# Kernel tuning notes

Hardware: AMD Instinct MI355X
Metric: run time of the kernel (lower is better)

The kernel has to match this reference:

```python
import jax, jax.numpy as jnp
import numpy as np

NUM_GRAPHS = 128
NODES_PER_GRAPH = 512
N_NODES = NUM_GRAPHS * NODES_PER_GRAPH
N_EDGES = 524288
IN_DIM = 128
HID = 128
OUT_DIM = 10
N_LAYERS = 3
POOL_RATIO = 0.5  # TopKPooling default ratio


def setup_inputs() -> dict:
    key = jax.random.key(0)
    ks = jax.random.split(key, 16)
    x = jax.random.normal(ks[0], (N_NODES, IN_DIM), dtype=jnp.float32)
    edge_index = jax.random.randint(ks[1], (2, N_EDGES), 0, N_NODES, dtype=jnp.int64)
    batch = jnp.repeat(jnp.arange(NUM_GRAPHS, dtype=jnp.int64), NODES_PER_GRAPH)
    s = 0.05
    return {
        "x": x,
        "edge_index": edge_index,
        "batch": batch,
        "emb_W": jax.random.normal(ks[2], (IN_DIM, HID), dtype=jnp.float32) * s,
        "emb_b": jnp.zeros((HID,), dtype=jnp.float32),
        "gcn_W": jax.random.normal(ks[3], (N_LAYERS, HID, HID), dtype=jnp.float32) * s,
        "gcn_b": jnp.zeros((N_LAYERS, HID), dtype=jnp.float32),
        "pool_p": jax.random.normal(ks[4], (HID,), dtype=jnp.float32),
        "fc1_W": jax.random.normal(ks[5], (HID, 128), dtype=jnp.float32) * s,
        "fc1_b": jnp.zeros((128,), dtype=jnp.float32),
        "fc2_W": jax.random.normal(ks[6], (128, 64), dtype=jnp.float32) * s,
        "fc2_b": jnp.zeros((64,), dtype=jnp.float32),
        "fc3_W": jax.random.normal(ks[7], (64, OUT_DIM), dtype=jnp.float32) * s,
        "fc3_b": jnp.zeros((OUT_DIM,), dtype=jnp.float32),
    }


def reference(x, edge_index, batch, emb_W, emb_b, gcn_W, gcn_b, pool_p,
              fc1_W, fc1_b, fc2_W, fc2_b, fc3_W, fc3_b):
    n = x.shape[0]
    # embedding
    h = x @ emb_W + emb_b
    # GCNConv normalization (PyG semantics): add self loops, deg from target scatter
    loop = jnp.arange(n, dtype=edge_index.dtype)
    src = jnp.concatenate([edge_index[0], loop])
    dst = jnp.concatenate([edge_index[1], loop])
    deg = jax.ops.segment_sum(jnp.ones_like(src, dtype=h.dtype), dst, num_segments=n)
    dinv = jnp.where(deg > 0, jax.lax.rsqrt(jnp.maximum(deg, 1e-12)), 0.0)
    norm = dinv[src] * dinv[dst]  # [E+n]
    for l in range(gcn_W.shape[0]):
        hw = h @ gcn_W[l]                                   # [n, HID]
        msg = hw[src] * norm[:, None]                        # gather + scale
        h = jax.nn.relu(jax.ops.segment_sum(msg, dst, num_segments=n) + gcn_b[l])
    # TopKPooling (ratio=0.5, tanh nonlinearity), uniform graphs -> reshape + top_k
    npg = n // NUM_GRAPHS
    k = int(np.ceil(POOL_RATIO * npg))
    score = (h @ pool_p) / jnp.linalg.norm(pool_p)           # [n]
    score_g = score.reshape(NUM_GRAPHS, npg)
    topv, topi = jax.lax.top_k(score_g, k)                   # [G, k]
    h_g = h.reshape(NUM_GRAPHS, npg, -1)
    h_sel = jnp.take_along_axis(h_g, topi[:, :, None], axis=1) * jnp.tanh(topv)[:, :, None]
    pooled = h_sel.mean(axis=1)                              # global_mean_pool -> [G, HID]
    # MLP head (dropout is identity in eval)
    z = jax.nn.relu(pooled @ fc1_W + fc1_b)
    z = jax.nn.relu(z @ fc2_W + fc2_b)
    return z @ fc3_W + fc3_b
```

## Files before the change

kernel.cpp:

```cpp
#include <hip/hip_runtime.h>
#include <hip/hip_bf16.h>
#include <math.h>


static __device__ __forceinline__ float4 f4add(float4 a, float4 b) {
    return make_float4(a.x + b.x, a.y + b.y, a.z + b.z, a.w + b.w);
}
static __device__ __forceinline__ float4 f4fma(float s, float4 a, float4 acc) {
    return make_float4(fmaf(s, a.x, acc.x), fmaf(s, a.y, acc.y),
                       fmaf(s, a.z, acc.z), fmaf(s, a.w, acc.w));
}

__global__ __launch_bounds__(128) void fold_emb(
    const float* __restrict__ embW, const float* __restrict__ embb,
    const float* __restrict__ W0, float* __restrict__ W01,
    float* __restrict__ b01)
{
    const int r = blockIdx.x;
    const int c = threadIdx.x;
    __shared__ float rs[128];
    rs[c] = (r < 128) ? embW[r * 128 + c] : embb[c];
    __syncthreads();
    float s = 0.f;
#pragma unroll 8
    for (int k = 0; k < 128; k++) s = fmaf(rs[k], W0[k * 128 + c], s);
    if (r < 128) W01[r * 128 + c] = s;
    else         b01[c] = s;
}

#define ASTRIDE 260
#define WSTRIDE 140
__global__ __launch_bounds__(256) void gemm128(
    const float* __restrict__ A, const float* __restrict__ W,
    const float* __restrict__ bias, const float* __restrict__ rowscale,
    float* __restrict__ out, int n)
{
    __shared__ float As[32 * ASTRIDE];
    __shared__ float Ws[32 * WSTRIDE];
    const int tid  = threadIdx.x;
    const int rb   = blockIdx.x * 256;
    const int tc   = tid & 15;
    const int tr   = tid >> 4;
    const int colg = tc * 8;
    const int cswz = colg + ((colg >> 5) << 2);
    const int rowg = tr * 16;

    const int a_kq = tid & 7;
    const int a_r0 = tid >> 3;
    const int w_c  = (tid & 31) * 4;
    const int w_cs = w_c + ((w_c >> 5) << 2);
    const int w_k  = tid >> 5;

    float acc[16][8];
#pragma unroll
    for (int i = 0; i < 16; i++)
#pragma unroll
        for (int j = 0; j < 8; j++) acc[i][j] = 0.f;

    float4 areg[8], wreg[4];
#pragma unroll
    for (int t = 0; t < 8; t++)
        areg[t] = *(const float4*)&A[(size_t)(rb + t * 32 + a_r0) * 128 + a_kq * 4];
#pragma unroll
    for (int t = 0; t < 4; t++)
        wreg[t] = *(const float4*)&W[(size_t)(t * 8 + w_k) * 128 + w_c];

#pragma unroll 1
    for (int k0 = 0; k0 < 128; k0 += 32) {
#pragma unroll
        for (int t = 0; t < 8; t++) {
            const int m = t * 32 + a_r0;
            const float4 av = areg[t];
            As[(a_kq * 4 + 0) * ASTRIDE + m] = av.x;
            As[(a_kq * 4 + 1) * ASTRIDE + m] = av.y;
            As[(a_kq * 4 + 2) * ASTRIDE + m] = av.z;
            As[(a_kq * 4 + 3) * ASTRIDE + m] = av.w;
        }
#pragma unroll
        for (int t = 0; t < 4; t++)
            *(float4*)&Ws[(t * 8 + w_k) * WSTRIDE + w_cs] = wreg[t];
        __syncthreads();
        if (k0 < 96) {
#pragma unroll
            for (int t = 0; t < 8; t++)
                areg[t] = *(const float4*)&A[(size_t)(rb + t * 32 + a_r0) * 128 + k0 + 32 + a_kq * 4];
#pragma unroll
            for (int t = 0; t < 4; t++)
                wreg[t] = *(const float4*)&W[(size_t)(k0 + 32 + t * 8 + w_k) * 128 + w_c];
        }
#pragma unroll 8
        for (int kk = 0; kk < 32; kk++) {
            const float* ar = &As[kk * ASTRIDE + rowg];
            float4 a0 = *(const float4*)&ar[0];
            float4 a1 = *(const float4*)&ar[4];
            float4 a2 = *(const float4*)&ar[8];
            float4 a3 = *(const float4*)&ar[12];
            float4 b0 = *(const float4*)&Ws[kk * WSTRIDE + cswz];
            float4 b1 = *(const float4*)&Ws[kk * WSTRIDE + cswz + 4];
            float av[16] = {a0.x, a0.y, a0.z, a0.w, a1.x, a1.y, a1.z, a1.w,
                            a2.x, a2.y, a2.z, a2.w, a3.x, a3.y, a3.z, a3.w};
            float bv[8]  = {b0.x, b0.y, b0.z, b0.w, b1.x, b1.y, b1.z, b1.w};
#pragma unroll
            for (int i = 0; i < 16; i++)
#pragma unroll
                for (int j = 0; j < 8; j++) acc[i][j] = fmaf(av[i], bv[j], acc[i][j]);
        }
        __syncthreads();
    }

    float4 bb0 = make_float4(0.f, 0.f, 0.f, 0.f), bb1 = bb0;
    if (bias) {
        bb0 = *(const float4*)&bias[colg];
        bb1 = *(const float4*)&bias[colg + 4];
    }
#pragma unroll
    for (int i = 0; i < 16; i++) {
        const int row  = rb + rowg + i;
        const float sc = rowscale ? rowscale[row] : 1.f;
        float4 o0, o1;
        o0.x = (acc[i][0] + bb0.x) * sc;  o0.y = (acc[i][1] + bb0.y) * sc;
        o0.z = (acc[i][2] + bb0.z) * sc;  o0.w = (acc[i][3] + bb0.w) * sc;
        o1.x = (acc[i][4] + bb1.x) * sc;  o1.y = (acc[i][5] + bb1.y) * sc;
        o1.z = (acc[i][6] + bb1.z) * sc;  o1.w = (acc[i][7] + bb1.w) * sc;
        *(float4*)&out[(size_t)row * 128 + colg]     = o0;
        *(float4*)&out[(size_t)row * 128 + colg + 4] = o1;
    }
}

__global__ void count_edges(const int* __restrict__ dst, int* __restrict__ cnt, int E)
{
    int e = blockIdx.x * blockDim.x + threadIdx.x;
    if (e < E) atomicAdd(&cnt[dst[e]], 1);
}

__global__ void dinv_k(const int* __restrict__ cnt, float* __restrict__ dinv, int n)
{
    int i = blockIdx.x * blockDim.x + threadIdx.x;
    if (i < n) dinv[i] = rsqrtf((float)(cnt[i] + 1));
}

__global__ void scan1(const int* __restrict__ cnt, int* __restrict__ offs,
                      int* __restrict__ bsum)
{
    __shared__ int tmp[256];
    int t = threadIdx.x;
    int i = blockIdx.x * 256 + t;
    int v = cnt[i];
    tmp[t] = v;
    __syncthreads();
    for (int o = 1; o < 256; o <<= 1) {
        int add = (t >= o) ? tmp[t - o] : 0;
        __syncthreads();
        tmp[t] += add;
        __syncthreads();
    }
    offs[i] = tmp[t] - v;
    if (t == 255) bsum[blockIdx.x] = tmp[255];
}

__global__ void scan2(const int* __restrict__ bsum, int* __restrict__ boff)
{
    __shared__ int tmp[256];
    int t = threadIdx.x;
    int v = bsum[t];
    tmp[t] = v;
    __syncthreads();
    for (int o = 1; o < 256; o <<= 1) {
        int add = (t >= o) ? tmp[t - o] : 0;
        __syncthreads();
        tmp[t] += add;
        __syncthreads();
    }
    boff[t] = tmp[t] - v;
}

__global__ void scan3(int* __restrict__ offs, const int* __restrict__ boff,
                      int* __restrict__ cursor, int n, int E)
{
    int i = blockIdx.x * 256 + threadIdx.x;
    int v = offs[i] + boff[blockIdx.x];
    offs[i]   = v;
    cursor[i] = v;
    if (i == 0) offs[n] = E;
}

__global__ void scatter_edges(const int* __restrict__ src, const int* __restrict__ dst,
                              int* __restrict__ cursor, int* __restrict__ csr, int E)
{
    int e = blockIdx.x * blockDim.x + threadIdx.x;
    if (e < E) {
        int d   = dst[e];
        int pos = atomicAdd(&cursor[d], 1);
        csr[pos] = src[e];
    }
}

__global__ __launch_bounds__(256) void aggregate(
    const float* __restrict__ hs, const int* __restrict__ csr,
    const int* __restrict__ offs, const float* __restrict__ dinv,
    const float* __restrict__ bias, float* __restrict__ hout,
    const float* __restrict__ pool_p, float* __restrict__ scores, int n)
{
    const int grp  = threadIdx.x >> 5;
    const int lane = threadIdx.x & 31;
    const int node = blockIdx.x * 8 + grp;
    const float4* __restrict__ hv = (const float4*)hs;

    const int e0 = offs[node], e1 = offs[node + 1];

    int   ix[16];
    float mk[16];
#pragma unroll
    for (int j = 0; j < 16; j++) {
        const int  e  = e0 + j;
        const bool v  = e < e1;
        const int  ce = v ? e : (e1 > 0 ? e1 - 1 : 0);
        ix[j] = csr[ce];
        mk[j] = v ? 1.f : 0.f;
    }

    float4 a0 = hv[(size_t)node * 32 + lane];
    float4 a1 = make_float4(0.f, 0.f, 0.f, 0.f);
    float4 a2 = a1, a3 = a1;

#pragma unroll
    for (int b = 0; b < 2; b++) {
        float4 r[8];
#pragma unroll
        for (int j = 0; j < 8; j++)
            r[j] = hv[(size_t)ix[b * 8 + j] * 32 + lane];
        a0 = f4fma(mk[b * 8 + 0], r[0], a0);
        a1 = f4fma(mk[b * 8 + 1], r[1], a1);
        a2 = f4fma(mk[b * 8 + 2], r[2], a2);
        a3 = f4fma(mk[b * 8 + 3], r[3], a3);
        a0 = f4fma(mk[b * 8 + 4], r[4], a0);
        a1 = f4fma(mk[b * 8 + 5], r[5], a1);
        a2 = f4fma(mk[b * 8 + 6], r[6], a2);
        a3 = f4fma(mk[b * 8 + 7], r[7], a3);
    }
    for (int e = e0 + 16; e < e1; e++) {
        a1 = f4add(a1, hv[(size_t)csr[e] * 32 + lane]);
    }

    float4 s = f4add(f4add(a0, a1), f4add(a2, a3));
    const float dv = dinv[node];
    const float4 bb = ((const float4*)bias)[lane];
    float4 o;
    o.x = fmaxf(fmaf(s.x, dv, bb.x), 0.f);
    o.y = fmaxf(fmaf(s.y, dv, bb.y), 0.f);
    o.z = fmaxf(fmaf(s.z, dv, bb.z), 0.f);
    o.w = fmaxf(fmaf(s.w, dv, bb.w), 0.f);
    ((float4*)hout)[(size_t)node * 32 + lane] = o;

    if (scores) {
        float4 pv = ((const float4*)pool_p)[lane];
        float d  = o.x * pv.x + o.y * pv.y + o.z * pv.z + o.w * pv.w;
        float nn = pv.x * pv.x + pv.y * pv.y + pv.z * pv.z + pv.w * pv.w;
#pragma unroll
        for (int off = 16; off > 0; off >>= 1) {
            d  += __shfl_xor(d, off);
            nn += __shfl_xor(nn, off);
        }
        if (lane == 0) scores[node] = d * rsqrtf(nn);
    }
}

__global__ __launch_bounds__(512) void topk_pool(
    const float* __restrict__ scores, const float* __restrict__ h,
    float* __restrict__ pooled)
{
    __shared__ float s[512];
    __shared__ int   sel[256];
    __shared__ float w[256];
    __shared__ float4 red[512];
    const int g = blockIdx.x;
    const int i = threadIdx.x;
    s[i] = scores[g * 512 + i];
    __syncthreads();
    float si = s[i];
    int rank = 0;
    for (int j = 0; j < 512; j++) {
        float sj = s[j];
        rank += (sj > si) || (sj == si && j < i);
    }
    if (rank < 256) {
        sel[rank] = i;
        w[rank]   = tanhf(si) * (1.f / 256.f);
    }
    __syncthreads();
    const int c   = (i & 31) * 4;
    const int grp = i >> 5;
    float4 acc = make_float4(0.f, 0.f, 0.f, 0.f);
    for (int t = grp; t < 256; t += 16) {
        float wt  = w[t];
        int   idx = sel[t];
        float4 r = *(const float4*)&h[((size_t)g * 512 + idx) * 128 + c];
        acc = f4fma(wt, r, acc);
    }
    red[i] = acc;
    __syncthreads();
    if (i < 256) red[i] = f4add(red[i], red[i + 256]);
    __syncthreads();
    if (i < 128) red[i] = f4add(red[i], red[i + 128]);
    __syncthreads();
    if (i < 64) red[i] = f4add(red[i], red[i + 64]);
    __syncthreads();
    if (i < 32) {
        float4 v = f4add(red[i], red[i + 32]);
        *(float4*)&pooled[g * 128 + i * 4] = v;
    }
}

__global__ __launch_bounds__(128) void mlp_head(
    const float* __restrict__ pooled,
    const float* __restrict__ fc1W, const float* __restrict__ fc1b,
    const float* __restrict__ fc2W, const float* __restrict__ fc2b,
    const float* __restrict__ fc3W, const float* __restrict__ fc3b,
    float* __restrict__ out)
{
    __shared__ float pld[128];
    __shared__ float z1[128];
    __shared__ float z2[64];
    int g = blockIdx.x, j = threadIdx.x;
    pld[j] = pooled[g * 128 + j];
    __syncthreads();
    float a = fc1b[j];
    for (int k = 0; k < 128; k++) a += pld[k] * fc1W[k * 128 + j];
    z1[j] = fmaxf(a, 0.f);
    __syncthreads();
    if (j < 64) {
        float b = fc2b[j];
        for (int k = 0; k < 128; k++) b += z1[k] * fc2W[k * 64 + j];
        z2[j] = fmaxf(b, 0.f);
    }
    __syncthreads();
    if (j < 10) {
        float o = fc3b[j];
        for (int k = 0; k < 64; k++) o += z2[k] * fc3W[k * 10 + j];
        out[g * 10 + j] = o;
    }
}

extern "C" void kernel_launch(void* const* d_in, const int* in_sizes, int n_in,
                              void* d_out, int out_size, void* d_ws, size_t ws_size,
                              hipStream_t stream)
{
    const float* x     = (const float*)d_in[0];
    const int*   eidx  = (const int*)d_in[1];
    const float* embW  = (const float*)d_in[3];
    const float* embb  = (const float*)d_in[4];
    const float* gcnW  = (const float*)d_in[5];
    const float* gcnb  = (const float*)d_in[6];
    const float* poolp = (const float*)d_in[7];
    const float* fc1W  = (const float*)d_in[8];
    const float* fc1b  = (const float*)d_in[9];
    const float* fc2W  = (const float*)d_in[10];
    const float* fc2b  = (const float*)d_in[11];
    const float* fc3W  = (const float*)d_in[12];
    const float* fc3b  = (const float*)d_in[13];
    float* out = (float*)d_out;

    const int n = in_sizes[0] / 128;
    const int E = in_sizes[1] / 2;
    const int G = n / 512;

    const int* src = eidx;
    const int* dst = eidx + E;

    char* ws = (char*)d_ws;
    size_t off = 0;
    auto carve = [&](size_t bytes) {
        void* p = ws + off;
        off += (bytes + 255) & ~(size_t)255;
        return p;
    };
    float* h      = (float*)carve((size_t)n * 128 * 4);
    float* hs     = (float*)carve((size_t)n * 128 * 4);
    float* dinv   = (float*)carve((size_t)n * 4);
    int*   cnt    = (int*)carve((size_t)n * 4);
    int*   offs   = (int*)carve((size_t)(n + 1) * 4);
    int*   cursor = (int*)carve((size_t)n * 4);
    int*   bsum   = (int*)carve(256 * 4);
    int*   boff   = (int*)carve(256 * 4);
    int*   csr    = (int*)carve((size_t)E * 4);
    float* scores = (float*)carve((size_t)n * 4);
    float* pooled = (float*)carve((size_t)G * 128 * 4);
    float* W01    = (float*)carve(128 * 128 * 4);
    float* b01    = (float*)carve(128 * 4);
    (void)ws_size;

    hipMemsetAsync(cnt, 0, (size_t)n * 4, stream);
    count_edges<<<E / 256, 256, 0, stream>>>(dst, cnt, E);
    dinv_k<<<n / 256, 256, 0, stream>>>(cnt, dinv, n);
    scan1<<<n / 256, 256, 0, stream>>>(cnt, offs, bsum);
    scan2<<<1, 256, 0, stream>>>(bsum, boff);
    scan3<<<n / 256, 256, 0, stream>>>(offs, boff, cursor, n, E);
    scatter_edges<<<E / 256, 256, 0, stream>>>(src, dst, cursor, csr, E);

    fold_emb<<<129, 128, 0, stream>>>(embW, embb, gcnW, W01, b01);

    gemm128<<<n / 256, 256, 0, stream>>>(x, W01, b01, dinv, hs, n);
    aggregate<<<n / 8, 256, 0, stream>>>(hs, csr, offs, dinv, gcnb, h,
                                         poolp, nullptr, n);

    for (int l = 1; l < 3; l++) {
        gemm128<<<n / 256, 256, 0, stream>>>(h, gcnW + (size_t)l * 128 * 128,
                                             nullptr, dinv, hs, n);
        aggregate<<<n / 8, 256, 0, stream>>>(
            hs, csr, offs, dinv, gcnb + (size_t)l * 128, h,
            poolp, (l == 2) ? scores : nullptr, n);
    }

    topk_pool<<<G, 512, 0, stream>>>(scores, h, pooled);
    mlp_head<<<G, 128, 0, stream>>>(pooled, fc1W, fc1b, fc2W, fc2b, fc3W, fc3b, out);
}
```

Baseline: 436.0 us.

## Halve GEMM row tile, fuse dinv into scan, and batch all aggregate gathers

The node GEMM tile drops from 256 to 128 rows per block, with 8x8 accumulators per thread, which doubles the block count and cuts register pressure for better occupancy and load balance. The A-tile LDS stride changes to 257, so the float4 LDS reads are no longer 16-byte aligned and may be split or rely on unaligned LDS support. The separate dinv kernel is folded into scan1, removing one launch and one read of the degree array. The aggregate kernel now issues all 16 neighbour gathers before any accumulation, raising memory-level parallelism at the cost of more live registers.

```diff
diff --git a/kernel.cpp b/kernel.cpp
--- a/kernel.cpp
+++ b/kernel.cpp
@@ -28,7 +28,7 @@
     else         b01[c] = s;
 }
 
-#define ASTRIDE 260
+#define ASTRIDE 257
 #define WSTRIDE 140
 __global__ __launch_bounds__(256) void gemm128(
     const float* __restrict__ A, const float* __restrict__ W,
@@ -38,29 +38,29 @@
     __shared__ float As[32 * ASTRIDE];
     __shared__ float Ws[32 * WSTRIDE];
     const int tid  = threadIdx.x;
-    const int rb   = blockIdx.x * 256;
+    const int rb   = blockIdx.x * 128;
     const int tc   = tid & 15;
     const int tr   = tid >> 4;
     const int colg = tc * 8;
     const int cswz = colg + ((colg >> 5) << 2);
-    const int rowg = tr * 16;
+    const int rowg = tr * 8;
 
     const int a_kq = tid & 7;
-    const int a_r0 = tid >> 3;
+    const int a_m  = tid >> 3;
     const int w_c  = (tid & 31) * 4;
     const int w_cs = w_c + ((w_c >> 5) << 2);
     const int w_k  = tid >> 5;
 
-    float acc[16][8];
-#pragma unroll
-    for (int i = 0; i < 16; i++)
+    float acc[8][8];
+#pragma unroll
+    for (int i = 0; i < 8; i++)
 #pragma unroll
         for (int j = 0; j < 8; j++) acc[i][j] = 0.f;
 
-    float4 areg[8], wreg[4];
-#pragma unroll
-    for (int t = 0; t < 8; t++)
-        areg[t] = *(const float4*)&A[(size_t)(rb + t * 32 + a_r0) * 128 + a_kq * 4];
+    float4 areg[4], wreg[4];
+#pragma unroll
+    for (int t = 0; t < 4; t++)
+        areg[t] = *(const float4*)&A[(size_t)(rb + t * 32 + a_m) * 128 + a_kq * 4];
 #pragma unroll
     for (int t = 0; t < 4; t++)
         wreg[t] = *(const float4*)&W[(size_t)(t * 8 + w_k) * 128 + w_c];
@@ -68,8 +68,8 @@
 #pragma unroll 1
     for (int k0 = 0; k0 < 128; k0 += 32) {
 #pragma unroll
-        for (int t = 0; t < 8; t++) {
-            const int m = t * 32 + a_r0;
+        for (int t = 0; t < 4; t++) {
+            const int m = t * 32 + a_m;
             const float4 av = areg[t];
             As[(a_kq * 4 + 0) * ASTRIDE + m] = av.x;
             As[(a_kq * 4 + 1) * ASTRIDE + m] = av.y;
@@ -82,26 +82,22 @@
         __syncthreads();
         if (k0 < 96) {
 #pragma unroll
-            for (int t = 0; t < 8; t++)
-                areg[t] = *(const float4*)&A[(size_t)(rb + t * 32 + a_r0) * 128 + k0 + 32 + a_kq * 4];
+            for (int t = 0; t < 4; t++)
+                areg[t] = *(const float4*)&A[(size_t)(rb + t * 32 + a_m) * 128 + k0 + 32 + a_kq * 4];
 #pragma unroll
             for (int t = 0; t < 4; t++)
                 wreg[t] = *(const float4*)&W[(size_t)(k0 + 32 + t * 8 + w_k) * 128 + w_c];
         }
 #pragma unroll 8
         for (int kk = 0; kk < 32; kk++) {
-            const float* ar = &As[kk * ASTRIDE + rowg];
-            float4 a0 = *(const float4*)&ar[0];
-            float4 a1 = *(const float4*)&ar[4];
-            float4 a2 = *(const float4*)&ar[8];
-            float4 a3 = *(const float4*)&ar[12];
+            float4 a0 = *(const float4*)&As[kk * ASTRIDE + rowg];
+            float4 a1 = *(const float4*)&As[kk * ASTRIDE + rowg + 4];
             float4 b0 = *(const float4*)&Ws[kk * WSTRIDE + cswz];
             float4 b1 = *(const float4*)&Ws[kk * WSTRIDE + cswz + 4];
-            float av[16] = {a0.x, a0.y, a0.z, a0.w, a1.x, a1.y, a1.z, a1.w,
-                            a2.x, a2.y, a2.z, a2.w, a3.x, a3.y, a3.z, a3.w};
-            float bv[8]  = {b0.x, b0.y, b0.z, b0.w, b1.x, b1.y, b1.z, b1.w};
-#pragma unroll
-            for (int i = 0; i < 16; i++)
+            float av[8] = {a0.x, a0.y, a0.z, a0.w, a1.x, a1.y, a1.z, a1.w};
+            float bv[8] = {b0.x, b0.y, b0.z, b0.w, b1.x, b1.y, b1.z, b1.w};
+#pragma unroll
+            for (int i = 0; i < 8; i++)
 #pragma unroll
                 for (int j = 0; j < 8; j++) acc[i][j] = fmaf(av[i], bv[j], acc[i][j]);
         }
@@ -114,7 +110,7 @@
         bb1 = *(const float4*)&bias[colg + 4];
     }
 #pragma unroll
-    for (int i = 0; i < 16; i++) {
+    for (int i = 0; i < 8; i++) {
         const int row  = rb + rowg + i;
         const float sc = rowscale ? rowscale[row] : 1.f;
         float4 o0, o1;
@@ -133,19 +129,14 @@
     if (e < E) atomicAdd(&cnt[dst[e]], 1);
 }
 
-__global__ void dinv_k(const int* __restrict__ cnt, float* __restrict__ dinv, int n)
-{
-    int i = blockIdx.x * blockDim.x + threadIdx.x;
-    if (i < n) dinv[i] = rsqrtf((float)(cnt[i] + 1));
-}
-
 __global__ void scan1(const int* __restrict__ cnt, int* __restrict__ offs,
-                      int* __restrict__ bsum)
+                      int* __restrict__ bsum, float* __restrict__ dinv)
 {
     __shared__ int tmp[256];
     int t = threadIdx.x;
     int i = blockIdx.x * 256 + t;
     int v = cnt[i];
+    dinv[i] = rsqrtf((float)(v + 1));
     tmp[t] = v;
     __syncthreads();
     for (int o = 1; o < 256; o <<= 1) {
@@ -219,24 +210,22 @@
         mk[j] = v ? 1.f : 0.f;
     }
 
-    float4 a0 = hv[(size_t)node * 32 + lane];
+    float4 self = hv[(size_t)node * 32 + lane];
+    float4 r[16];
+#pragma unroll
+    for (int j = 0; j < 16; j++)
+        r[j] = hv[(size_t)ix[j] * 32 + lane];
+    asm volatile("" ::: "memory");
+
+    float4 a0 = self;
     float4 a1 = make_float4(0.f, 0.f, 0.f, 0.f);
     float4 a2 = a1, a3 = a1;
-
-#pragma unroll
-    for (int b = 0; b < 2; b++) {
-        float4 r[8];
-#pragma unroll
-        for (int j = 0; j < 8; j++)
-            r[j] = hv[(size_t)ix[b * 8 + j] * 32 + lane];
-        a0 = f4fma(mk[b * 8 + 0], r[0], a0);
-        a1 = f4fma(mk[b * 8 + 1], r[1], a1);
-        a2 = f4fma(mk[b * 8 + 2], r[2], a2);
-        a3 = f4fma(mk[b * 8 + 3], r[3], a3);
-        a0 = f4fma(mk[b * 8 + 4], r[4], a0);
-        a1 = f4fma(mk[b * 8 + 5], r[5], a1);
-        a2 = f4fma(mk[b * 8 + 6], r[6], a2);
-        a3 = f4fma(mk[b * 8 + 7], r[7], a3);
+#pragma unroll
+    for (int j = 0; j < 16; j += 4) {
+        a0 = f4fma(mk[j + 0], r[j + 0], a0);
+        a1 = f4fma(mk[j + 1], r[j + 1], a1);
+        a2 = f4fma(mk[j + 2], r[j + 2], a2);
+        a3 = f4fma(mk[j + 3], r[j + 3], a3);
     }
     for (int e = e0 + 16; e < e1; e++) {
         a1 = f4add(a1, hv[(size_t)csr[e] * 32 + lane]);
@@ -391,20 +380,19 @@
 
     hipMemsetAsync(cnt, 0, (size_t)n * 4, stream);
     count_edges<<<E / 256, 256, 0, stream>>>(dst, cnt, E);
-    dinv_k<<<n / 256, 256, 0, stream>>>(cnt, dinv, n);
-    scan1<<<n / 256, 256, 0, stream>>>(cnt, offs, bsum);
+    scan1<<<n / 256, 256, 0, stream>>>(cnt, offs, bsum, dinv);
     scan2<<<1, 256, 0, stream>>>(bsum, boff);
     scan3<<<n / 256, 256, 0, stream>>>(offs, boff, cursor, n, E);
     scatter_edges<<<E / 256, 256, 0, stream>>>(src, dst, cursor, csr, E);
 
     fold_emb<<<129, 128, 0, stream>>>(embW, embb, gcnW, W01, b01);
 
-    gemm128<<<n / 256, 256, 0, stream>>>(x, W01, b01, dinv, hs, n);
+    gemm128<<<n / 128, 256, 0, stream>>>(x, W01, b01, dinv, hs, n);
     aggregate<<<n / 8, 256, 0, stream>>>(hs, csr, offs, dinv, gcnb, h,
                                          poolp, nullptr, n);
 
     for (int l = 1; l < 3; l++) {
-        gemm128<<<n / 256, 256, 0, stream>>>(h, gcnW + (size_t)l * 128 * 128,
+        gemm128<<<n / 128, 256, 0, stream>>>(h, gcnW + (size_t)l * 128 * 128,
                                              nullptr, dinv, hs, n);
         aggregate<<<n / 8, 256, 0, stream>>>(
             hs, csr, offs, dinv, gcnb + (size_t)l * 128, h,
```

After: 430.5 us. Within noise of the previous version (-1.3%).
